# Kernel optimization log

Measured on AMD Instinct MI355X. Metric: run time of the kernel, lower is better.

Reference implementation:

```python
import math
import jax, jax.numpy as jnp
import numpy as np

B, S, H, D = 2, 2048, 16, 64

def setup_inputs() -> dict:
    key = jax.random.key(0)
    qkv = jax.random.normal(key, (B, S, 3, H, D), dtype=jnp.float32)
    return {"qkv": qkv}

def reference(qkv) -> jnp.ndarray:
    # qkv: [B, S, 3, H, D]
    q = qkv[:, :, 0]  # [B, S, H, D]
    k = qkv[:, :, 1]
    v = qkv[:, :, 2]
    seqlen = qkv.shape[1]
    softmax_scale = 1.0 / math.sqrt(q.shape[-1])
    # scores: [B, H, T, S]
    scores = jnp.einsum('bthd,bshd->bhts', q, k * softmax_scale)
    # additive causal mask with -10000 above the diagonal (matches torch.triu(..., 1))
    causal_mask = jnp.triu(jnp.full((seqlen, seqlen), -10000.0, dtype=scores.dtype), 1)
    scores = scores + causal_mask
    attention = jax.nn.softmax(scores, axis=-1)
    # dropout_p = 0.0 (eval), so no dropout applied
    output = jnp.einsum('bhts,bshd->bthd', attention, v)  # [B, T, H, D]
    return output
```

## Files before the change

kernel.cpp:

```cpp
#include <hip/hip_runtime.h>

typedef __bf16 bf16x8 __attribute__((ext_vector_type(8)));
typedef float f32x4 __attribute__((ext_vector_type(4)));

constexpr int Bc = 2, Sc = 2048, Hc = 16, Dc = 64;
constexpr int QBLK = 64, KVBLK = 64;
constexpr int NT = Sc / QBLK;
constexpr int ROWSTR = 3 * Hc * Dc;


__global__ __launch_bounds__(256)
void fattn_kernel(const float* __restrict__ qkv, float* __restrict__ out) {
  const int xlow  = blockIdx.x;
  const int xhigh = NT - 1 - xlow;
  const int bh = blockIdx.y;
  const int b = bh >> 4, h = bh & 15;

  const int tid  = threadIdx.x;
  const int wave = tid >> 6;
  const int lane = tid & 63;
  const int lg = lane >> 4;
  const int li = lane & 15;

  const float* qp = qkv + (size_t)b * Sc * ROWSTR + h * Dc;
  const float* kp = qp + Hc * Dc;
  const float* vp = qp + 2 * Hc * Dc;

  __shared__ __align__(16) char k_s[KVBLK * Dc * 2];
  __shared__ __align__(16) char vt_s[Dc * KVBLK * 2];
  __shared__ __align__(16) char pl_s[4][16 * KVBLK * 2];
  char* pw = pl_s[wave];

  const int qwL = xlow * QBLK + wave * 16;
  const int qwH = xhigh * QBLK + wave * 16;
  bf16x8 qfL[2], qfH[2];
  {
    const float* qrL = qp + (size_t)(qwL + li) * ROWSTR + 8 * lg;
    const float* qrH = qp + (size_t)(qwH + li) * ROWSTR + 8 * lg;
#pragma unroll
    for (int fi = 0; fi < 2; ++fi) {
      f32x4 a0 = *(const f32x4*)(qrL + 32 * fi);
      f32x4 a1 = *(const f32x4*)(qrL + 32 * fi + 4);
      f32x4 b0 = *(const f32x4*)(qrH + 32 * fi);
      f32x4 b1 = *(const f32x4*)(qrH + 32 * fi + 4);
      bf16x8 qa, qb;
#pragma unroll
      for (int j = 0; j < 4; ++j) {
        qa[j] = (__bf16)(a0[j] * 0.125f); qa[j + 4] = (__bf16)(a1[j] * 0.125f);
        qb[j] = (__bf16)(b0[j] * 0.125f); qb[j + 4] = (__bf16)(b1[j] * 0.125f);
      }
      qfL[fi] = qa; qfH[fi] = qb;
    }
  }

  f32x4 oL[4], oH[4];
  float mLr[4], lLr[4], mHr[4], lHr[4];
#pragma unroll
  for (int n = 0; n < 4; ++n) { oL[n] = f32x4{0,0,0,0}; oH[n] = f32x4{0,0,0,0}; }
#pragma unroll
  for (int r = 0; r < 4; ++r) { mLr[r] = -1e30f; lLr[r] = 0.f; mHr[r] = -1e30f; lHr[r] = 0.f; }

  auto tile_step = [&](int kv0, bool diag, int qw, bf16x8* qf,
                       f32x4* oacc, float* mrow, float* lrow) {
    f32x4 sacc[4];
#pragma unroll
    for (int n = 0; n < 4; ++n) sacc[n] = f32x4{0, 0, 0, 0};
    __builtin_amdgcn_s_setprio(1);
#pragma unroll
    for (int n = 0; n < 4; ++n) {
      const int krow = 16 * n + li;
#pragma unroll
      for (int fi = 0; fi < 2; ++fi) {
        const int kb_byte = (krow * 128 + fi * 64 + lg * 16) ^ ((krow & 7) << 4);
        bf16x8 kb = *(const bf16x8*)(k_s + kb_byte);
        sacc[n] = __builtin_amdgcn_mfma_f32_16x16x32_bf16(qf[fi], kb, sacc[n], 0, 0, 0);
      }
    }
    __builtin_amdgcn_s_setprio(0);

    if (diag) {
#pragma unroll
      for (int n = 0; n < 4; ++n)
#pragma unroll
        for (int r = 0; r < 4; ++r)
          if (kv0 + 16 * n + li > qw + 4 * lg + r) sacc[n][r] = -1e30f;
    }

    float pm[4];
#pragma unroll
    for (int r = 0; r < 4; ++r)
      pm[r] = fmaxf(fmaxf(sacc[0][r], sacc[1][r]), fmaxf(sacc[2][r], sacc[3][r]));
#pragma unroll
    for (int msk = 1; msk <= 8; msk <<= 1)
#pragma unroll
      for (int r = 0; r < 4; ++r)
        pm[r] = fmaxf(pm[r], __shfl_xor(pm[r], msk, 64));

    float scl[4], lsum[4];
#pragma unroll
    for (int r = 0; r < 4; ++r) {
      float mnew = fmaxf(mrow[r], pm[r]);
      scl[r] = __expf(mrow[r] - mnew);
      mrow[r] = mnew;
      lsum[r] = 0.f;
    }
#pragma unroll
    for (int n = 0; n < 4; ++n)
#pragma unroll
      for (int r = 0; r < 4; ++r) {
        float p = __expf(sacc[n][r] - mrow[r]);
        sacc[n][r] = p;
        lsum[r] += p;
      }
#pragma unroll
    for (int msk = 1; msk <= 8; msk <<= 1)
#pragma unroll
      for (int r = 0; r < 4; ++r)
        lsum[r] += __shfl_xor(lsum[r], msk, 64);
#pragma unroll
    for (int r = 0; r < 4; ++r) lrow[r] = lrow[r] * scl[r] + lsum[r];
#pragma unroll
    for (int n = 0; n < 4; ++n)
#pragma unroll
      for (int r = 0; r < 4; ++r) oacc[n][r] *= scl[r];

#pragma unroll
    for (int n = 0; n < 4; ++n)
#pragma unroll
      for (int r = 0; r < 4; ++r) {
        const int row = 4 * lg + r;
        const int col = 16 * n + li;
        int byte = (row * KVBLK + col) * 2;
        byte ^= (row & 7) << 4;
        *(__bf16*)(pw + byte) = (__bf16)sacc[n][r];
      }

    __builtin_amdgcn_s_setprio(1);
#pragma unroll
    for (int ks = 0; ks < 2; ++ks) {
      int pbyte = (li * KVBLK + 32 * ks + 8 * lg) * 2;
      pbyte ^= (li & 7) << 4;
      bf16x8 pa = *(const bf16x8*)(pw + pbyte);
#pragma unroll
      for (int n = 0; n < 4; ++n) {
        const int row = 16 * n + li;
        int vbyte = (row * KVBLK + 32 * ks + 8 * lg) * 2;
        vbyte ^= (row & 7) << 4;
        bf16x8 vb = *(const bf16x8*)(vt_s + vbyte);
        oacc[n] = __builtin_amdgcn_mfma_f32_16x16x32_bf16(pa, vb, oacc[n], 0, 0, 0);
      }
    }
    __builtin_amdgcn_s_setprio(0);
  };

  for (int t = 0; t <= xhigh; ++t) {
    const int kv0 = t * KVBLK;

#pragma unroll
    for (int it = 0; it < 2; ++it) {
      const int u = tid + it * 256;
      const int r = u >> 3, g = u & 7;
      const float* ksrc = kp + (size_t)(kv0 + r) * ROWSTR + g * 8;
      f32x4 k0 = *(const f32x4*)ksrc;
      f32x4 k1 = *(const f32x4*)(ksrc + 4);
      bf16x8 kb;
#pragma unroll
      for (int j = 0; j < 4; ++j) { kb[j] = (__bf16)k0[j]; kb[j + 4] = (__bf16)k1[j]; }
      int kbyte = (r * 128 + g * 16) ^ ((r & 7) << 4);
      *(bf16x8*)(k_s + kbyte) = kb;

      const float* vsrc = vp + (size_t)(kv0 + r) * ROWSTR + g * 8;
      f32x4 v0 = *(const f32x4*)vsrc;
      f32x4 v1 = *(const f32x4*)(vsrc + 4);
#pragma unroll
      for (int j = 0; j < 8; ++j) {
        const int d = g * 8 + j;
        const float val = (j < 4) ? v0[j] : v1[j - 4];
        int vbyte = (d * 128 + r * 2) ^ ((d & 7) << 4);
        *(__bf16*)(vt_s + vbyte) = (__bf16)val;
      }
    }
    __syncthreads();

    tile_step(kv0, t == xhigh, qwH, qfH, oH, mHr, lHr);
    if (t <= xlow)
      tile_step(kv0, t == xlow, qwL, qfL, oL, mLr, lLr);

    __syncthreads();
  }

#pragma unroll
  for (int r = 0; r < 4; ++r) {
    const float invH = 1.0f / lHr[r];
    const float invL = 1.0f / lLr[r];
    float* opH = out + ((size_t)(b * Sc + qwH + 4 * lg + r) * Hc + h) * Dc;
    float* opL = out + ((size_t)(b * Sc + qwL + 4 * lg + r) * Hc + h) * Dc;
#pragma unroll
    for (int n = 0; n < 4; ++n) {
      opH[16 * n + li] = oH[n][r] * invH;
      opL[16 * n + li] = oL[n][r] * invL;
    }
  }
}

extern "C" void kernel_launch(void* const* d_in, const int* in_sizes, int n_in,
                              void* d_out, int out_size, void* d_ws, size_t ws_size,
                              hipStream_t stream) {
  const float* qkv = (const float*)d_in[0];
  float* out = (float*)d_out;
  dim3 grid(NT / 2, Bc * Hc);
  fattn_kernel<<<grid, 256, 0, stream>>>(qkv, out);
}
```

Before: 98.96 us.

## Double-buffer K/V tiles with register prefetch and lazy softmax rescaling

Adds double-buffered K/V shared memory, prefetching the next tile's global loads into registers while the current tile computes, so each iteration needs one barrier instead of two. It also folds log2(e) into the Q scale to use exp2, skips the running-max rescale unless the max grows by more than a threshold, and writes packed bf16 pairs for the V transpose and the P tile via lane shuffles. It adds a block-index swizzle, separate P buffers for the two query tiles, and a launch bound of two blocks per CU. The costs are more registers and shared memory, plus a small numeric risk from the lazy rescaling.

```diff
diff --git a/kernel.cpp b/kernel.cpp
--- a/kernel.cpp
+++ b/kernel.cpp
@@ -2,21 +2,31 @@
 
 typedef __bf16 bf16x8 __attribute__((ext_vector_type(8)));
 typedef float f32x4 __attribute__((ext_vector_type(4)));
+typedef unsigned int u32;
 
 constexpr int Bc = 2, Sc = 2048, Hc = 16, Dc = 64;
 constexpr int QBLK = 64, KVBLK = 64;
 constexpr int NT = Sc / QBLK;
 constexpr int ROWSTR = 3 * Hc * Dc;
-
-
-__global__ __launch_bounds__(256)
+constexpr float QSCALE = 0.125f * 1.4426950408889634f;
+
+
+static __device__ __forceinline__ u32 pack2(float a, float b) {
+  unsigned short x = __builtin_bit_cast(unsigned short, (__bf16)a);
+  unsigned short y = __builtin_bit_cast(unsigned short, (__bf16)b);
+  return (u32)x | ((u32)y << 16);
+}
+
+__global__ __launch_bounds__(256, 2)
 void fattn_kernel(const float* __restrict__ qkv, float* __restrict__ out) {
-  const int xlow  = blockIdx.x;
+  const int id = blockIdx.x + blockIdx.y * gridDim.x;
+  const int swz = (id & 7) * 64 + (id >> 3);
+  const int xlow = swz & 15;
   const int xhigh = NT - 1 - xlow;
-  const int bh = blockIdx.y;
+  const int bh = swz >> 4;
   const int b = bh >> 4, h = bh & 15;
 
-  const int tid  = threadIdx.x;
+  const int tid = threadIdx.x;
   const int wave = tid >> 6;
   const int lane = tid & 63;
   const int lg = lane >> 4;
@@ -26,10 +36,11 @@
   const float* kp = qp + Hc * Dc;
   const float* vp = qp + 2 * Hc * Dc;
 
-  __shared__ __align__(16) char k_s[KVBLK * Dc * 2];
-  __shared__ __align__(16) char vt_s[Dc * KVBLK * 2];
-  __shared__ __align__(16) char pl_s[4][16 * KVBLK * 2];
-  char* pw = pl_s[wave];
+  __shared__ __align__(16) char k_s[2][KVBLK * Dc * 2];
+  __shared__ __align__(16) char v_s[2][Dc * KVBLK * 2];
+  __shared__ __align__(16) char p_s[4][2][16 * KVBLK * 2];
+  char* pw_H = &p_s[wave][0][0];
+  char* pw_L = &p_s[wave][1][0];
 
   const int qwL = xlow * QBLK + wave * 16;
   const int qwH = xhigh * QBLK + wave * 16;
@@ -46,8 +57,8 @@
       bf16x8 qa, qb;
 #pragma unroll
       for (int j = 0; j < 4; ++j) {
-        qa[j] = (__bf16)(a0[j] * 0.125f); qa[j + 4] = (__bf16)(a1[j] * 0.125f);
-        qb[j] = (__bf16)(b0[j] * 0.125f); qb[j + 4] = (__bf16)(b1[j] * 0.125f);
+        qa[j] = (__bf16)(a0[j] * QSCALE); qa[j + 4] = (__bf16)(a1[j] * QSCALE);
+        qb[j] = (__bf16)(b0[j] * QSCALE); qb[j + 4] = (__bf16)(b1[j] * QSCALE);
       }
       qfL[fi] = qa; qfH[fi] = qb;
     }
@@ -56,137 +67,182 @@
   f32x4 oL[4], oH[4];
   float mLr[4], lLr[4], mHr[4], lHr[4];
 #pragma unroll
-  for (int n = 0; n < 4; ++n) { oL[n] = f32x4{0,0,0,0}; oH[n] = f32x4{0,0,0,0}; }
+  for (int n = 0; n < 4; ++n) { oL[n] = f32x4{0, 0, 0, 0}; oH[n] = f32x4{0, 0, 0, 0}; }
 #pragma unroll
   for (int r = 0; r < 4; ++r) { mLr[r] = -1e30f; lLr[r] = 0.f; mHr[r] = -1e30f; lHr[r] = 0.f; }
 
-  auto tile_step = [&](int kv0, bool diag, int qw, bf16x8* qf,
-                       f32x4* oacc, float* mrow, float* lrow) {
+  f32x4 kr[4], vr[4];
+  auto stage_load = [&](int kv0) {
+#pragma unroll
+    for (int it = 0; it < 2; ++it) {
+      const int u = tid + it * 256, r = u >> 3, g = u & 7;
+      const float* ks = kp + (size_t)(kv0 + r) * ROWSTR + g * 8;
+      const float* vs = vp + (size_t)(kv0 + r) * ROWSTR + g * 8;
+      kr[2 * it]     = *(const f32x4*)ks;
+      kr[2 * it + 1] = *(const f32x4*)(ks + 4);
+      vr[2 * it]     = *(const f32x4*)vs;
+      vr[2 * it + 1] = *(const f32x4*)(vs + 4);
+    }
+  };
+  auto stage_write = [&](char* kd, char* vd) {
+#pragma unroll
+    for (int it = 0; it < 2; ++it) {
+      const int u = tid + it * 256, r = u >> 3, g = u & 7;
+      bf16x8 kb;
+#pragma unroll
+      for (int j = 0; j < 4; ++j) {
+        kb[j] = (__bf16)kr[2 * it][j]; kb[j + 4] = (__bf16)kr[2 * it + 1][j];
+      }
+      *(bf16x8*)(kd + ((r * 128 + g * 16) ^ ((r & 7) << 4))) = kb;
+
+      const int odd = r & 1;
+      f32x4 tmp = odd ? vr[2 * it] : vr[2 * it + 1];
+      f32x4 rcv;
+#pragma unroll
+      for (int j = 0; j < 4; ++j) rcv[j] = __shfl_xor(tmp[j], 8, 64);
+      const int kvb2 = (r & ~1) * 2;
+#pragma unroll
+      for (int s = 0; s < 4; ++s) {
+        const int dj = (s + g) & 3;
+        const float lo = odd ? rcv[dj] : vr[2 * it][dj];
+        const float hi = odd ? vr[2 * it + 1][dj] : rcv[dj];
+        const int d = 8 * g + 4 * odd + dj;
+        *(u32*)(vd + ((d * 128 + kvb2) ^ ((d & 7) << 4))) = pack2(lo, hi);
+      }
+    }
+  };
+
+  auto tile_step = [&](const bf16x8 (&kf)[4][2], const bf16x8* qf, f32x4* oacc,
+                       float* mrow, float* lrow, char* pw, const char* vt,
+                       bool diag, int kv0, int qw) {
     f32x4 sacc[4];
 #pragma unroll
     for (int n = 0; n < 4; ++n) sacc[n] = f32x4{0, 0, 0, 0};
     __builtin_amdgcn_s_setprio(1);
 #pragma unroll
+    for (int n = 0; n < 4; ++n)
+#pragma unroll
+      for (int fi = 0; fi < 2; ++fi)
+        sacc[n] = __builtin_amdgcn_mfma_f32_16x16x32_bf16(qf[fi], kf[n][fi], sacc[n], 0, 0, 0);
+    __builtin_amdgcn_s_setprio(0);
+
+    if (diag) {
+      const int qrow = qw + 4 * lg;
+#pragma unroll
+      for (int n = 0; n < 4; ++n)
+#pragma unroll
+        for (int r = 0; r < 4; ++r)
+          if (kv0 + 16 * n + li > qrow + r) sacc[n][r] = -1e30f;
+    }
+
+    float pm[4];
+#pragma unroll
+    for (int r = 0; r < 4; ++r)
+      pm[r] = fmaxf(fmaxf(sacc[0][r], sacc[1][r]), fmaxf(sacc[2][r], sacc[3][r]));
+#pragma unroll
+    for (int msk = 1; msk <= 8; msk <<= 1)
+#pragma unroll
+      for (int r = 0; r < 4; ++r)
+        pm[r] = fmaxf(pm[r], __shfl_xor(pm[r], msk, 64));
+
+    bool need = false;
+#pragma unroll
+    for (int r = 0; r < 4; ++r) need = need || (pm[r] > mrow[r] + 8.0f);
+    if (__any(need)) {
+#pragma unroll
+      for (int r = 0; r < 4; ++r) {
+        float mnew = fmaxf(mrow[r], pm[r]);
+        float scl = __builtin_exp2f(mrow[r] - mnew);
+        mrow[r] = mnew;
+        lrow[r] *= scl;
+#pragma unroll
+        for (int n = 0; n < 4; ++n) oacc[n][r] *= scl;
+      }
+    }
+
+    float lsum[4] = {0.f, 0.f, 0.f, 0.f};
+#pragma unroll
+    for (int n = 0; n < 4; ++n)
+#pragma unroll
+      for (int r = 0; r < 4; ++r) {
+        float p = __builtin_exp2f(sacc[n][r] - mrow[r]);
+        sacc[n][r] = p;
+        lsum[r] += p;
+      }
+#pragma unroll
+    for (int msk = 1; msk <= 8; msk <<= 1)
+#pragma unroll
+      for (int r = 0; r < 4; ++r)
+        lsum[r] += __shfl_xor(lsum[r], msk, 64);
+#pragma unroll
+    for (int r = 0; r < 4; ++r) lrow[r] += lsum[r];
+
+    {
+      const int oddli = li & 1;
+      const int kvoff = (li & ~1) * 2;
+      const int q0 = 4 * lg + 2 * oddli;
+      const int sw0 = (q0 & 7) << 4;
+      const int sw1 = ((q0 + 1) & 7) << 4;
+#pragma unroll
+      for (int n = 0; n < 4; ++n) {
+        float t0 = oddli ? sacc[n][0] : sacc[n][2];
+        float t1 = oddli ? sacc[n][1] : sacc[n][3];
+        float r0 = __shfl_xor(t0, 1, 64);
+        float r1 = __shfl_xor(t1, 1, 64);
+        float lo0 = oddli ? r0 : sacc[n][0];
+        float hi0 = oddli ? sacc[n][2] : r0;
+        float lo1 = oddli ? r1 : sacc[n][1];
+        float hi1 = oddli ? sacc[n][3] : r1;
+        const int base = n * 32 + kvoff;
+        *(u32*)(pw + ((q0 * 128 + base) ^ sw0)) = pack2(lo0, hi0);
+        *(u32*)(pw + (((q0 + 1) * 128 + base) ^ sw1)) = pack2(lo1, hi1);
+      }
+    }
+
+#pragma unroll
+    for (int ks = 0; ks < 2; ++ks) {
+      const int pbyte = (li * 128 + (32 * ks + 8 * lg) * 2) ^ ((li & 7) << 4);
+      bf16x8 pa = *(const bf16x8*)(pw + pbyte);
+      __builtin_amdgcn_s_setprio(1);
+#pragma unroll
+      for (int n = 0; n < 4; ++n) {
+        const int row = 16 * n + li;
+        const int vbyte = (row * 128 + (32 * ks + 8 * lg) * 2) ^ ((row & 7) << 4);
+        bf16x8 vb = *(const bf16x8*)(vt + vbyte);
+        oacc[n] = __builtin_amdgcn_mfma_f32_16x16x32_bf16(pa, vb, oacc[n], 0, 0, 0);
+      }
+      __builtin_amdgcn_s_setprio(0);
+    }
+  };
+
+  stage_load(0);
+  stage_write(k_s[0], v_s[0]);
+  __syncthreads();
+
+  int cur = 0;
+  for (int t = 0; t <= xhigh; ++t) {
+    const int kv0 = t * KVBLK;
+    const bool have_next = (t < xhigh);
+    if (have_next) stage_load(kv0 + KVBLK);
+
+    const char* ksrc = k_s[cur];
+    bf16x8 kf[4][2];
+#pragma unroll
     for (int n = 0; n < 4; ++n) {
       const int krow = 16 * n + li;
-#pragma unroll
-      for (int fi = 0; fi < 2; ++fi) {
-        const int kb_byte = (krow * 128 + fi * 64 + lg * 16) ^ ((krow & 7) << 4);
-        bf16x8 kb = *(const bf16x8*)(k_s + kb_byte);
-        sacc[n] = __builtin_amdgcn_mfma_f32_16x16x32_bf16(qf[fi], kb, sacc[n], 0, 0, 0);
-      }
-    }
-    __builtin_amdgcn_s_setprio(0);
-
-    if (diag) {
-#pragma unroll
-      for (int n = 0; n < 4; ++n)
-#pragma unroll
-        for (int r = 0; r < 4; ++r)
-          if (kv0 + 16 * n + li > qw + 4 * lg + r) sacc[n][r] = -1e30f;
-    }
-
-    float pm[4];
-#pragma unroll
-    for (int r = 0; r < 4; ++r)
-      pm[r] = fmaxf(fmaxf(sacc[0][r], sacc[1][r]), fmaxf(sacc[2][r], sacc[3][r]));
-#pragma unroll
-    for (int msk = 1; msk <= 8; msk <<= 1)
-#pragma unroll
-      for (int r = 0; r < 4; ++r)
-        pm[r] = fmaxf(pm[r], __shfl_xor(pm[r], msk, 64));
-
-    float scl[4], lsum[4];
-#pragma unroll
-    for (int r = 0; r < 4; ++r) {
-      float mnew = fmaxf(mrow[r], pm[r]);
-      scl[r] = __expf(mrow[r] - mnew);
-      mrow[r] = mnew;
-      lsum[r] = 0.f;
-    }
-#pragma unroll
-    for (int n = 0; n < 4; ++n)
-#pragma unroll
-      for (int r = 0; r < 4; ++r) {
-        float p = __expf(sacc[n][r] - mrow[r]);
-        sacc[n][r] = p;
-        lsum[r] += p;
-      }
-#pragma unroll
-    for (int msk = 1; msk <= 8; msk <<= 1)
-#pragma unroll
-      for (int r = 0; r < 4; ++r)
-        lsum[r] += __shfl_xor(lsum[r], msk, 64);
-#pragma unroll
-    for (int r = 0; r < 4; ++r) lrow[r] = lrow[r] * scl[r] + lsum[r];
-#pragma unroll
-    for (int n = 0; n < 4; ++n)
-#pragma unroll
-      for (int r = 0; r < 4; ++r) oacc[n][r] *= scl[r];
-
-#pragma unroll
-    for (int n = 0; n < 4; ++n)
-#pragma unroll
-      for (int r = 0; r < 4; ++r) {
-        const int row = 4 * lg + r;
-        const int col = 16 * n + li;
-        int byte = (row * KVBLK + col) * 2;
-        byte ^= (row & 7) << 4;
-        *(__bf16*)(pw + byte) = (__bf16)sacc[n][r];
-      }
-
-    __builtin_amdgcn_s_setprio(1);
-#pragma unroll
-    for (int ks = 0; ks < 2; ++ks) {
-      int pbyte = (li * KVBLK + 32 * ks + 8 * lg) * 2;
-      pbyte ^= (li & 7) << 4;
-      bf16x8 pa = *(const bf16x8*)(pw + pbyte);
-#pragma unroll
-      for (int n = 0; n < 4; ++n) {
-        const int row = 16 * n + li;
-        int vbyte = (row * KVBLK + 32 * ks + 8 * lg) * 2;
-        vbyte ^= (row & 7) << 4;
-        bf16x8 vb = *(const bf16x8*)(vt_s + vbyte);
-        oacc[n] = __builtin_amdgcn_mfma_f32_16x16x32_bf16(pa, vb, oacc[n], 0, 0, 0);
-      }
-    }
-    __builtin_amdgcn_s_setprio(0);
-  };
-
-  for (int t = 0; t <= xhigh; ++t) {
-    const int kv0 = t * KVBLK;
-
-#pragma unroll
-    for (int it = 0; it < 2; ++it) {
-      const int u = tid + it * 256;
-      const int r = u >> 3, g = u & 7;
-      const float* ksrc = kp + (size_t)(kv0 + r) * ROWSTR + g * 8;
-      f32x4 k0 = *(const f32x4*)ksrc;
-      f32x4 k1 = *(const f32x4*)(ksrc + 4);
-      bf16x8 kb;
-#pragma unroll
-      for (int j = 0; j < 4; ++j) { kb[j] = (__bf16)k0[j]; kb[j + 4] = (__bf16)k1[j]; }
-      int kbyte = (r * 128 + g * 16) ^ ((r & 7) << 4);
-      *(bf16x8*)(k_s + kbyte) = kb;
-
-      const float* vsrc = vp + (size_t)(kv0 + r) * ROWSTR + g * 8;
-      f32x4 v0 = *(const f32x4*)vsrc;
-      f32x4 v1 = *(const f32x4*)(vsrc + 4);
-#pragma unroll
-      for (int j = 0; j < 8; ++j) {
-        const int d = g * 8 + j;
-        const float val = (j < 4) ? v0[j] : v1[j - 4];
-        int vbyte = (d * 128 + r * 2) ^ ((d & 7) << 4);
-        *(__bf16*)(vt_s + vbyte) = (__bf16)val;
-      }
-    }
+      const int sw = (krow & 7) << 4;
+#pragma unroll
+      for (int fi = 0; fi < 2; ++fi)
+        kf[n][fi] = *(const bf16x8*)(ksrc + ((krow * 128 + fi * 64 + lg * 16) ^ sw));
+    }
+
+    tile_step(kf, qfH, oH, mHr, lHr, pw_H, v_s[cur], t == xhigh, kv0, qwH);
+    if (t <= xlow)
+      tile_step(kf, qfL, oL, mLr, lLr, pw_L, v_s[cur], t == xlow, kv0, qwL);
+
+    if (have_next) stage_write(k_s[cur ^ 1], v_s[cur ^ 1]);
     __syncthreads();
-
-    tile_step(kv0, t == xhigh, qwH, qfH, oH, mHr, lHr);
-    if (t <= xlow)
-      tile_step(kv0, t == xlow, qwL, qfL, oL, mLr, lLr);
-
-    __syncthreads();
+    cur ^= 1;
   }
 
 #pragma unroll
```

New measurement: 145.8 us. 1.47x slower.
